# Optimization experiments

Hardware: AMD Instinct MI355X
Metric: run time of the kernel (lower is better)

## Reference

```python
import jax, jax.numpy as jnp
import numpy as np
from jax.nn import relu, softplus, sigmoid

B, T, C, L = 256, 128, 16, 64
ENC, H, OBS_IN, NLAGS = 32, 64, 8, 24
SUBSTEPS = 2


def setup_inputs() -> dict:
    key = jax.random.key(0)
    ks = jax.random.split(key, 32)
    rn = lambda k, shp, s=0.1: jax.random.normal(k, shp, dtype=jnp.float32) * s
    return {
        "timestamps": jnp.linspace(0.0, 1.0, T, dtype=jnp.float32),
        "obs": rn(ks[0], (B, NLAGS, OBS_IN), 1.0),
        "coef_d": rn(ks[1], (B, T - 1, C)),
        "coef_c": rn(ks[2], (B, T - 1, C)),
        "coef_b": rn(ks[3], (B, T - 1, C)),
        "coef_a": rn(ks[4], (B, T - 1, C)),
        "gru_wih": rn(ks[5], (3 * H, OBS_IN)),
        "gru_whh": rn(ks[6], (3 * H, H)),
        "gru_bih": rn(ks[7], (3 * H,)),
        "gru_bhh": rn(ks[8], (3 * H,)),
        "gru_lin_w": rn(ks[9], (ENC, H)),
        "ie_w0": rn(ks[10], (128, ENC + C)),
        "ie_b0": rn(ks[11], (128,)),
        "ie_wh": rn(ks[12], (1, 128, 128)),
        "ie_bh": rn(ks[13], (1, 128)),
        "ie_wout": rn(ks[14], (L, 128)),
        "ie_bout": rn(ks[15], (L,)),
        "vf_w0": rn(ks[16], (128, L)),
        "vf_b0": rn(ks[17], (128,)),
        "vf_wh": rn(ks[18], (1, 128, 128)),
        "vf_bh": rn(ks[19], (1, 128)),
        "vf_wout": rn(ks[20], (L * C, 128)),
        "vf_bout": rn(ks[21], (L * C,)),
        "dec_w0": rn(ks[22], (L // 2, L)),
        "dec_b0": rn(ks[23], (L // 2,)),
        "dec_wh": rn(ks[24], (1, L // 2, L // 2)),
        "dec_bh": rn(ks[25], (1, L // 2)),
        "dec_wout": rn(ks[26], (8, L // 2)),
        "dec_bout": rn(ks[27], (8,)),
    }


def _mlp(x, w0, b0, wh, bh, wout, bout, act, fact):
    h = act(w0 @ x + b0)
    for i in range(wh.shape[0]):  # fixed small depth
        h = act(wh[i] @ h + bh[i])
    return fact(wout @ h + bout)


_ident = lambda v: v


def reference(timestamps, obs, coef_d, coef_c, coef_b, coef_a,
              gru_wih, gru_whh, gru_bih, gru_bhh, gru_lin_w,
              ie_w0, ie_b0, ie_wh, ie_bh, ie_wout, ie_bout,
              vf_w0, vf_b0, vf_wh, vf_bh, vf_wout, vf_bout,
              dec_w0, dec_b0, dec_wh, dec_bh, dec_wout, dec_bout):

    def single(obs_s, d_s, c_s, b_s, a_s):
        # --- GRU observation encoder ---
        def cell(h, x):
            gi = gru_wih @ x + gru_bih
            gh = gru_whh @ h + gru_bhh
            ir, iz, inn = jnp.split(gi, 3)
            hr, hz, hn = jnp.split(gh, 3)
            r = sigmoid(ir + hr)
            z = sigmoid(iz + hz)
            n = jnp.tanh(inn + r * hn)
            return (1.0 - z) * n + z * h, None
        hT, _ = jax.lax.scan(cell, jnp.zeros((H,), jnp.float32), obs_s)
        enc = gru_lin_w @ hT
        # control.evaluate(t0): cubic poly at frac=0 -> constant coeff a[0]
        x0 = a_s[0]
        y0 = _mlp(jnp.concatenate([enc, x0]), ie_w0, ie_b0, ie_wh, ie_bh, ie_wout, ie_bout, relu, _ident)

        def vf(y):
            return _mlp(y, vf_w0, vf_b0, vf_wh, vf_bh, vf_wout, vf_bout, softplus, jnp.tanh).reshape(L, C)

        js = jnp.arange(SUBSTEPS, dtype=jnp.float32)

        def interval(y, xs):
            t0, t1, di, ci, bi = xs
            hstep = (t1 - t0) / SUBSTEPS
            def f(frac, yy):
                dx = bi + 2.0 * ci * frac + 3.0 * di * frac * frac  # dX/dt on this interval
                return vf(yy) @ dx  # (L,)
            def sub(yy, j):  # one fixed Dopri5 step
                f0 = j * hstep
                k1 = f(f0, yy)
                k2 = f(f0 + hstep / 5, yy + hstep * (k1 / 5))
                k3 = f(f0 + 3 * hstep / 10, yy + hstep * (3 / 40 * k1 + 9 / 40 * k2))
                k4 = f(f0 + 4 * hstep / 5, yy + hstep * (44 / 45 * k1 - 56 / 15 * k2 + 32 / 9 * k3))
                k5 = f(f0 + 8 * hstep / 9, yy + hstep * (19372 / 6561 * k1 - 25360 / 2187 * k2 + 64448 / 6561 * k3 - 212 / 729 * k4))
                k6 = f(f0 + hstep, yy + hstep * (9017 / 3168 * k1 - 355 / 33 * k2 + 46732 / 5247 * k3 + 49 / 176 * k4 - 5103 / 18656 * k5))
                yn = yy + hstep * (35 / 384 * k1 + 500 / 1113 * k3 + 125 / 192 * k4 - 2187 / 6784 * k5 + 11 / 84 * k6)
                return yn, None
            y, _ = jax.lax.scan(jax.checkpoint(sub), y, js)
            return y, y

        xs = (timestamps[:-1], timestamps[1:], d_s, c_s, b_s)
        _, ys_rest = jax.lax.scan(interval, y0, xs)
        ys = jnp.concatenate([y0[None], ys_rest], axis=0)  # (T, L)
        dec = lambda yy: _mlp(yy, dec_w0, dec_b0, dec_wh, dec_bh, dec_wout, dec_bout, relu, _ident)
        return jax.vmap(dec)(ys)  # (T, state_size)

    return jax.vmap(single)(obs, coef_d, coef_c, coef_b, coef_a)  # (B, T, state_size)
```

## Files before the change

kernel.cpp:

```cpp
#include <hip/hip_runtime.h>
#include <hip/hip_fp16.h>

#define TPB 512

typedef _Float16 h2v __attribute__((ext_vector_type(2)));

__device__ __forceinline__ float dot2f(unsigned int a, unsigned int b, float c) {
#if __has_builtin(__builtin_amdgcn_fdot2)
    return __builtin_amdgcn_fdot2(__builtin_bit_cast(h2v, a), __builtin_bit_cast(h2v, b), c, false);
#else
    float2 af = __half22float2(__builtin_bit_cast(__half2, a));
    float2 bf = __half22float2(__builtin_bit_cast(__half2, b));
    return fmaf(af.y, bf.y, fmaf(af.x, bf.x, c));
#endif
}

__device__ __forceinline__ unsigned int pack2(float a, float b) {
    unsigned int lo = (unsigned int)__half_as_ushort(__float2half_rn(a));
    unsigned int hi = (unsigned int)__half_as_ushort(__float2half_rn(b));
    return lo | (hi << 16);
}

__device__ __forceinline__ float softplus_f(float x) {
    return fmaxf(x, 0.f) + __logf(1.f + __expf(-fabsf(x)));
}
__device__ __forceinline__ float tanh_f(float x) {
    float e = __expf(2.f * x);
    return 1.f - 2.f / (e + 1.f);
}
__device__ __forceinline__ float sigmoid_f(float x) {
    return 1.f / (1.f + __expf(-x));
}

template <int CTRL>
__device__ __forceinline__ float dpp_add(float x) {
    int m = __builtin_amdgcn_update_dpp(0, __builtin_bit_cast(int, x), CTRL, 0xF, 0xF, true);
    return x + __builtin_bit_cast(float, m);
}

__device__ __forceinline__ float dot16(const float* w, const float* base) {
    float4 a = *reinterpret_cast<const float4*>(base);
    float4 b = *reinterpret_cast<const float4*>(base + 4);
    float4 c = *reinterpret_cast<const float4*>(base + 8);
    float4 d = *reinterpret_cast<const float4*>(base + 12);
    float s0 = w[0] * a.x, s1 = w[1] * a.y, s2 = w[2] * a.z, s3 = w[3] * a.w;
    s0 = fmaf(w[4], b.x, s0);
    s1 = fmaf(w[5], b.y, s1);
    s2 = fmaf(w[6], b.z, s2);
    s3 = fmaf(w[7], b.w, s3);
    s0 = fmaf(w[8], c.x, s0);
    s1 = fmaf(w[9], c.y, s1);
    s2 = fmaf(w[10], c.z, s2);
    s3 = fmaf(w[11], c.w, s3);
    s0 = fmaf(w[12], d.x, s0);
    s1 = fmaf(w[13], d.y, s1);
    s2 = fmaf(w[14], d.z, s2);
    s3 = fmaf(w[15], d.w, s3);
    return (s0 + s1) + (s2 + s3);
}

__global__ __launch_bounds__(TPB, 1) void ncde_kernel(
    const float* __restrict__ timestamps, const float* __restrict__ obs,
    const float* __restrict__ coef_d, const float* __restrict__ coef_c,
    const float* __restrict__ coef_b, const float* __restrict__ coef_a,
    const float* __restrict__ gru_wih, const float* __restrict__ gru_whh,
    const float* __restrict__ gru_bih, const float* __restrict__ gru_bhh,
    const float* __restrict__ gru_lin_w,
    const float* __restrict__ ie_w0, const float* __restrict__ ie_b0,
    const float* __restrict__ ie_wh, const float* __restrict__ ie_bh,
    const float* __restrict__ ie_wout, const float* __restrict__ ie_bout,
    const float* __restrict__ vf_w0, const float* __restrict__ vf_b0,
    const float* __restrict__ vf_wh, const float* __restrict__ vf_bh,
    const float* __restrict__ vf_wout, const float* __restrict__ vf_bout,
    const float* __restrict__ dec_w0, const float* __restrict__ dec_b0,
    const float* __restrict__ dec_wh, const float* __restrict__ dec_bh,
    const float* __restrict__ dec_wout, const float* __restrict__ dec_bout,
    float* __restrict__ out)
{
    const int b = blockIdx.x;
    const int tid = threadIdx.x;

    __shared__ __align__(16) float s_ysall[128][64];
    __shared__ __align__(16) float s_whh[192 * 65];
    __shared__ __align__(16) float s_wih[192 * 9];
    __shared__ __align__(16) float s_obs[24 * 8];
    __shared__ float s_gi[192];
    __shared__ float s_gh[192];
    __shared__ __align__(16) float s_y[64];
    __shared__ __align__(16) __half s_h1h[128];
    __shared__ __align__(16) __half s_h2h[128];
    __shared__ __align__(16) float s_k[6][64];
    __shared__ float s_bi[16], s_ci[16], s_di[16];
    __shared__ __align__(16) float s_v48[48];
    __shared__ float s_m1[128], s_m2[128];

    for (int idx = tid; idx < 192 * 64; idx += TPB)
        s_whh[(idx >> 6) * 65 + (idx & 63)] = gru_whh[idx];
    for (int idx = tid; idx < 192 * 8; idx += TPB)
        s_wih[(idx >> 3) * 9 + (idx & 7)] = gru_wih[idx];
    if (tid < 24 * 8) s_obs[tid] = obs[(size_t)b * 192 + tid];
    const float bih_r = (tid < 192) ? gru_bih[tid] : 0.f;
    const float bhh_r = (tid < 192) ? gru_bhh[tid] : 0.f;
    if (tid < 64) s_y[tid] = 0.f;
    __syncthreads();

    for (int step = 0; step < 24; ++step) {
        if (tid < 192) {
            float gi = bih_r;
            const float* wr = &s_wih[tid * 9];
            const float* xr = &s_obs[step * 8];
#pragma unroll
            for (int j = 0; j < 8; ++j) gi = fmaf(wr[j], xr[j], gi);
            float g0 = bhh_r, g1 = 0.f, g2 = 0.f, g3 = 0.f;
            const float* hr = &s_whh[tid * 65];
#pragma unroll 4
            for (int j = 0; j < 64; j += 4) {
                g0 = fmaf(hr[j + 0], s_y[j + 0], g0);
                g1 = fmaf(hr[j + 1], s_y[j + 1], g1);
                g2 = fmaf(hr[j + 2], s_y[j + 2], g2);
                g3 = fmaf(hr[j + 3], s_y[j + 3], g3);
            }
            s_gi[tid] = gi;
            s_gh[tid] = (g0 + g1) + (g2 + g3);
        }
        __syncthreads();
        if (tid < 64) {
            float rg = sigmoid_f(s_gi[tid] + s_gh[tid]);
            float zg = sigmoid_f(s_gi[64 + tid] + s_gh[64 + tid]);
            float ng = tanh_f(s_gi[128 + tid] + rg * s_gh[128 + tid]);
            s_y[tid] = (1.f - zg) * ng + zg * s_y[tid];
        }
        __syncthreads();
    }

    if (tid < 32) {
        float e = 0.f;
        const float* wr = gru_lin_w + tid * 64;
        for (int j = 0; j < 64; ++j) e = fmaf(wr[j], s_y[j], e);
        s_v48[tid] = e;
    } else if (tid < 48) {
        s_v48[tid] = coef_a[(size_t)b * 127 * 16 + (tid - 32)];
    }
    __syncthreads();

    if (tid < 128) {
        float a = ie_b0[tid];
        const float* wr = ie_w0 + tid * 48;
        for (int j = 0; j < 48; ++j) a = fmaf(wr[j], s_v48[j], a);
        s_m1[tid] = fmaxf(a, 0.f);
    }
    __syncthreads();
    if (tid < 128) {
        float a = ie_bh[tid];
        const float* wr = ie_wh + tid * 128;
        for (int j = 0; j < 128; ++j) a = fmaf(wr[j], s_m1[j], a);
        s_m2[tid] = fmaxf(a, 0.f);
    }
    __syncthreads();
    if (tid < 64) {
        float a = ie_bout[tid];
        const float* wr = ie_wout + tid * 128;
        for (int j = 0; j < 128; ++j) a = fmaf(wr[j], s_m2[j], a);
        s_y[tid] = a;
        s_ysall[0][tid] = a;
    }
    __syncthreads();

    const int row4 = tid >> 2, seg4 = tid & 3;
    float w0_r[16];
    {
        const float* base = vf_w0 + row4 * 64 + seg4 * 16;
#pragma unroll
        for (int j = 0; j < 16; ++j) w0_r[j] = base[j];
    }
    unsigned int wh_r[16];
    {
        const float* base = vf_wh + row4 * 128 + seg4 * 32;
#pragma unroll
        for (int j = 0; j < 16; ++j) wh_r[j] = pack2(base[2 * j], base[2 * j + 1]);
    }
    unsigned int wq0[64], wq1[64];
    {
        const float* r0 = vf_wout + (size_t)(2 * tid) * 128;
#pragma unroll
        for (int j = 0; j < 64; ++j) wq0[j] = pack2(r0[2 * j], r0[2 * j + 1]);
        const float* r1 = r0 + 128;
#pragma unroll
        for (int j = 0; j < 64; ++j) wq1[j] = pack2(r1[2 * j], r1[2 * j + 1]);
    }
    const float b0_r = vf_b0[row4];
    const float bh_r = vf_bh[row4];
    const float bo0 = vf_bout[2 * tid], bo1 = vf_bout[2 * tid + 1];
    const int l_idx = tid >> 3;
    const int c0 = 2 * (tid & 7);

    const size_t cofs = (size_t)b * 127 * 16;

#define VF_STAGE(S, ACC, CC)                                                   \
    do {                                                                       \
        {                                                                      \
            float acc_ = (ACC);                                                \
            acc_ = dpp_add<0xB1>(acc_);                                        \
            acc_ = dpp_add<0x4E>(acc_);                                        \
            if (seg4 == 0) s_h1h[row4] = __float2half_rn(softplus_f(acc_ + b0_r)); \
        }                                                                      \
        __syncthreads();                                                       \
        {                                                                      \
            const __half* hb = &s_h1h[seg4 * 32];                              \
            uint4 h0 = *reinterpret_cast<const uint4*>(hb);                    \
            uint4 h1v = *reinterpret_cast<const uint4*>(hb + 8);               \
            uint4 h2v2 = *reinterpret_cast<const uint4*>(hb + 16);             \
            uint4 h3 = *reinterpret_cast<const uint4*>(hb + 24);               \
            float a0 = dot2f(wh_r[0], h0.x, 0.f);                              \
            float a1 = dot2f(wh_r[1], h0.y, 0.f);                              \
            float a2 = dot2f(wh_r[2], h0.z, 0.f);                              \
            float a3 = dot2f(wh_r[3], h0.w, 0.f);                              \
            a0 = dot2f(wh_r[4], h1v.x, a0);                                    \
            a1 = dot2f(wh_r[5], h1v.y, a1);                                    \
            a2 = dot2f(wh_r[6], h1v.z, a2);                                    \
            a3 = dot2f(wh_r[7], h1v.w, a3);                                    \
            a0 = dot2f(wh_r[8], h2v2.x, a0);                                   \
            a1 = dot2f(wh_r[9], h2v2.y, a1);                                   \
            a2 = dot2f(wh_r[10], h2v2.z, a2);                                  \
            a3 = dot2f(wh_r[11], h2v2.w, a3);                                  \
            a0 = dot2f(wh_r[12], h3.x, a0);                                    \
            a1 = dot2f(wh_r[13], h3.y, a1);                                    \
            a2 = dot2f(wh_r[14], h3.z, a2);                                    \
            a3 = dot2f(wh_r[15], h3.w, a3);                                    \
            float a = (a0 + a1) + (a2 + a3);                                   \
            a = dpp_add<0xB1>(a);                                              \
            a = dpp_add<0x4E>(a);                                              \
            if (seg4 == 0) s_h2h[row4] = __float2half_rn(softplus_f(a + bh_r)); \
        }                                                                      \
        __syncthreads();                                                       \
        {                                                                      \
            float a0 = 0.f, a1 = 0.f, b0a = 0.f, b1a = 0.f;                    \
            _Pragma("unroll")                                                  \
            for (int k4 = 0; k4 < 16; ++k4) {                                  \
                uint4 hv = *reinterpret_cast<const uint4*>(&s_h2h[8 * k4]);    \
                a0 = dot2f(wq0[4 * k4 + 0], hv.x, a0);                         \
                b0a = dot2f(wq1[4 * k4 + 0], hv.x, b0a);                       \
                a1 = dot2f(wq0[4 * k4 + 1], hv.y, a1);                         \
                b1a = dot2f(wq1[4 * k4 + 1], hv.y, b1a);                       \
                a0 = dot2f(wq0[4 * k4 + 2], hv.z, a0);                         \
                b0a = dot2f(wq1[4 * k4 + 2], hv.z, b0a);                       \
                a1 = dot2f(wq0[4 * k4 + 3], hv.w, a1);                         \
                b1a = dot2f(wq1[4 * k4 + 3], hv.w, b1a);                       \
            }                                                                  \
            float v0 = tanh_f(a0 + a1 + bo0);                                  \
            float v1 = tanh_f(b0a + b1a + bo1);                                \
            float frac = fmaf((CC), hstep, f0);                                \
            float dx0 = fmaf(3.f * s_di[c0], frac * frac,                      \
                             fmaf(2.f * s_ci[c0], frac, s_bi[c0]));            \
            float dx1 = fmaf(3.f * s_di[c0 + 1], frac * frac,                  \
                             fmaf(2.f * s_ci[c0 + 1], frac, s_bi[c0 + 1]));    \
            float p = fmaf(v0, dx0, v1 * dx1);                                 \
            p = dpp_add<0xB1>(p);                                              \
            p = dpp_add<0x4E>(p);                                              \
            p = dpp_add<0x141>(p);   \
            if ((tid & 7) == 0) s_k[(S)][l_idx] = p;                           \
        }                                                                      \
        __syncthreads();                                                       \
    } while (0)

#pragma unroll 1
    for (int t = 0; t < 127; ++t) {
        if (tid < 16) s_bi[tid] = coef_b[cofs + t * 16 + tid];
        else if (tid < 32) s_ci[tid - 16] = coef_c[cofs + t * 16 + (tid - 16)];
        else if (tid < 48) s_di[tid - 32] = coef_d[cofs + t * 16 + (tid - 32)];
        const float t0 = timestamps[t], t1 = timestamps[t + 1];
        const float hstep = (t1 - t0) * 0.5f;

#pragma unroll 1
        for (int sub = 0; sub < 2; ++sub) {
            const float f0 = (float)sub * hstep;

            float ay = dot16(w0_r, &s_y[seg4 * 16]);
            VF_STAGE(0, ay, 0.f);
            float dk0 = dot16(w0_r, &s_k[0][seg4 * 16]);
            VF_STAGE(1, fmaf(hstep * 0.2f, dk0, ay), 0.2f);
            float dk1 = dot16(w0_r, &s_k[1][seg4 * 16]);
            VF_STAGE(2, fmaf(hstep, fmaf(3.f / 40.f, dk0, (9.f / 40.f) * dk1), ay), 0.3f);
            float dk2 = dot16(w0_r, &s_k[2][seg4 * 16]);
            VF_STAGE(3, fmaf(hstep, fmaf(44.f / 45.f, dk0,
                          fmaf(-56.f / 15.f, dk1, (32.f / 9.f) * dk2)), ay), 0.8f);
            float dk3 = dot16(w0_r, &s_k[3][seg4 * 16]);
            VF_STAGE(4, fmaf(hstep, fmaf(19372.f / 6561.f, dk0,
                          fmaf(-25360.f / 2187.f, dk1,
                          fmaf(64448.f / 6561.f, dk2, (-212.f / 729.f) * dk3))), ay),
                     8.f / 9.f);
            float dk4 = dot16(w0_r, &s_k[4][seg4 * 16]);
            VF_STAGE(5, fmaf(hstep, fmaf(9017.f / 3168.f, dk0,
                          fmaf(-355.f / 33.f, dk1,
                          fmaf(46732.f / 5247.f, dk2,
                          fmaf(49.f / 176.f, dk3, (-5103.f / 18656.f) * dk4)))), ay),
                     1.f);

            if (tid < 64) {
                float yv = s_y[tid];
                yv = fmaf(hstep * (35.f / 384.f), s_k[0][tid], yv);
                yv = fmaf(hstep * (500.f / 1113.f), s_k[2][tid], yv);
                yv = fmaf(hstep * (125.f / 192.f), s_k[3][tid], yv);
                yv = fmaf(hstep * (-2187.f / 6784.f), s_k[4][tid], yv);
                yv = fmaf(hstep * (11.f / 84.f), s_k[5][tid], yv);
                s_y[tid] = yv;
                if (sub == 1) s_ysall[t + 1][tid] = yv;
            }
            __syncthreads();
        }
    }

    const int wid = tid >> 6, lane = tid & 63;
    for (int t = wid; t < 128; t += 8) {
        const float* yy = s_ysall[t];
        float h1d = 0.f;
        if (lane < 32) {
            float a = dec_b0[lane];
            const float* wr = dec_w0 + lane * 64;
            for (int j = 0; j < 64; ++j) a = fmaf(wr[j], yy[j], a);
            h1d = fmaxf(a, 0.f);
        }
        float a2 = (lane < 32) ? dec_bh[lane] : 0.f;
#pragma unroll 8
        for (int j = 0; j < 32; ++j) {
            float hj = __shfl(h1d, j);
            if (lane < 32) a2 = fmaf(dec_wh[lane * 32 + j], hj, a2);
        }
        float h2d = fmaxf(a2, 0.f);
        float o = (lane < 8) ? dec_bout[lane] : 0.f;
#pragma unroll 8
        for (int j = 0; j < 32; ++j) {
            float hj = __shfl(h2d, j);
            if (lane < 8) o = fmaf(dec_wout[lane * 32 + j], hj, o);
        }
        if (lane < 8) out[(size_t)b * 1024 + t * 8 + lane] = o;
    }
}

extern "C" void kernel_launch(void* const* d_in, const int* in_sizes, int n_in,
                              void* d_out, int out_size, void* d_ws, size_t ws_size,
                              hipStream_t stream) {
    const float* p[29];
    for (int i = 0; i < 29; ++i) p[i] = (const float*)d_in[i];
    ncde_kernel<<<256, TPB, 0, stream>>>(
        p[0], p[1], p[2], p[3], p[4], p[5], p[6], p[7], p[8], p[9], p[10],
        p[11], p[12], p[13], p[14], p[15], p[16], p[17], p[18], p[19], p[20],
        p[21], p[22], p[23], p[24], p[25], p[26], p[27], p[28],
        (float*)d_out);
}
```

Before: 2.293 ms.

## Move half of vf_wout weights to LDS and decode per timestep inline

Half of the packed fp16 vector-field output weights (wq1) now live in a 128KB shared-memory pool instead of registers, reusing the GRU staging area, to cut register pressure and possible spills. The pool aliases the GRU scratch buffers, and the per-interval trajectory buffer is removed; the decoder MLP now runs on wave 0 right after each interval, between the integration steps. This trades register use for an extra LDS load per inner dot-product loop and puts decoder work on the serial critical path.

```diff
diff --git a/kernel.cpp b/kernel.cpp
--- a/kernel.cpp
+++ b/kernel.cpp
@@ -79,20 +79,24 @@
 {
     const int b = blockIdx.x;
     const int tid = threadIdx.x;
-
-    __shared__ __align__(16) float s_ysall[128][64];
-    __shared__ __align__(16) float s_whh[192 * 65];
-    __shared__ __align__(16) float s_wih[192 * 9];
-    __shared__ __align__(16) float s_obs[24 * 8];
-    __shared__ float s_gi[192];
-    __shared__ float s_gh[192];
+    const int lane = tid & 63, wv = tid >> 6;
+
+    __shared__ __align__(16) char s_pool[131072];
+    float* const s_whh = (float*)(s_pool);
+    float* const s_wih = (float*)(s_pool + 49920);
+    float* const s_obs = (float*)(s_pool + 56832);
+    float* const s_gi = (float*)(s_pool + 57600);
+    float* const s_gh = (float*)(s_pool + 58368);
+    float* const s_v48 = (float*)(s_pool + 59136);
+    float* const s_m1 = (float*)(s_pool + 59328);
+    float* const s_m2 = (float*)(s_pool + 59840);
+    unsigned* const s_wq1 = (unsigned*)(s_pool);
+
     __shared__ __align__(16) float s_y[64];
     __shared__ __align__(16) __half s_h1h[128];
     __shared__ __align__(16) __half s_h2h[128];
     __shared__ __align__(16) float s_k[6][64];
     __shared__ float s_bi[16], s_ci[16], s_di[16];
-    __shared__ __align__(16) float s_v48[48];
-    __shared__ float s_m1[128], s_m2[128];
 
     for (int idx = tid; idx < 192 * 64; idx += TPB)
         s_whh[(idx >> 6) * 65 + (idx & 63)] = gru_whh[idx];
@@ -162,7 +166,6 @@
         const float* wr = ie_wout + tid * 128;
         for (int j = 0; j < 128; ++j) a = fmaf(wr[j], s_m2[j], a);
         s_y[tid] = a;
-        s_ysall[0][tid] = a;
     }
     __syncthreads();
 
@@ -179,14 +182,23 @@
 #pragma unroll
         for (int j = 0; j < 16; ++j) wh_r[j] = pack2(base[2 * j], base[2 * j + 1]);
     }
-    unsigned int wq0[64], wq1[64];
+    unsigned int wq0[64];
     {
         const float* r0 = vf_wout + (size_t)(2 * tid) * 128;
 #pragma unroll
         for (int j = 0; j < 64; ++j) wq0[j] = pack2(r0[2 * j], r0[2 * j + 1]);
-        const float* r1 = r0 + 128;
-#pragma unroll
-        for (int j = 0; j < 64; ++j) wq1[j] = pack2(r1[2 * j], r1[2 * j + 1]);
+    }
+    {
+        const float* r1 = vf_wout + (size_t)(2 * tid + 1) * 128;
+#pragma unroll
+        for (int k4 = 0; k4 < 16; ++k4) {
+            uint4 wv1;
+            wv1.x = pack2(r1[8 * k4 + 0], r1[8 * k4 + 1]);
+            wv1.y = pack2(r1[8 * k4 + 2], r1[8 * k4 + 3]);
+            wv1.z = pack2(r1[8 * k4 + 4], r1[8 * k4 + 5]);
+            wv1.w = pack2(r1[8 * k4 + 6], r1[8 * k4 + 7]);
+            *reinterpret_cast<uint4*>(s_wq1 + (size_t)(k4 * 512 + tid) * 4) = wv1;
+        }
     }
     const float b0_r = vf_b0[row4];
     const float bh_r = vf_bh[row4];
@@ -195,6 +207,35 @@
     const int c0 = 2 * (tid & 7);
 
     const size_t cofs = (size_t)b * 127 * 16;
+    __syncthreads();
+
+    auto decode_t = [&](int t) {
+        if (wv == 0) {
+            float h1d = 0.f;
+            if (lane < 32) {
+                float a = dec_b0[lane];
+                const float* wr = dec_w0 + lane * 64;
+#pragma unroll 8
+                for (int j = 0; j < 64; ++j) a = fmaf(wr[j], s_y[j], a);
+                h1d = fmaxf(a, 0.f);
+            }
+            float a2 = (lane < 32) ? dec_bh[lane] : 0.f;
+#pragma unroll 8
+            for (int j = 0; j < 32; ++j) {
+                float hj = __shfl(h1d, j);
+                if (lane < 32) a2 = fmaf(dec_wh[lane * 32 + j], hj, a2);
+            }
+            float h2d = fmaxf(a2, 0.f);
+            float o = (lane < 8) ? dec_bout[lane] : 0.f;
+#pragma unroll 8
+            for (int j = 0; j < 32; ++j) {
+                float hj = __shfl(h2d, j);
+                if (lane < 8) o = fmaf(dec_wout[lane * 32 + j], hj, o);
+            }
+            if (lane < 8) out[(size_t)b * 1024 + t * 8 + lane] = o;
+        }
+    };
+    decode_t(0);
 
 #define VF_STAGE(S, ACC, CC)                                                   \
     do {                                                                       \
@@ -238,14 +279,15 @@
             _Pragma("unroll")                                                  \
             for (int k4 = 0; k4 < 16; ++k4) {                                  \
                 uint4 hv = *reinterpret_cast<const uint4*>(&s_h2h[8 * k4]);    \
+                uint4 wv1 = *reinterpret_cast<const uint4*>(s_wq1 + (k4 * 512 + tid) * 4); \
                 a0 = dot2f(wq0[4 * k4 + 0], hv.x, a0);                         \
-                b0a = dot2f(wq1[4 * k4 + 0], hv.x, b0a);                       \
+                b0a = dot2f(wv1.x, hv.x, b0a);                                 \
                 a1 = dot2f(wq0[4 * k4 + 1], hv.y, a1);                         \
-                b1a = dot2f(wq1[4 * k4 + 1], hv.y, b1a);                       \
+                b1a = dot2f(wv1.y, hv.y, b1a);                                 \
                 a0 = dot2f(wq0[4 * k4 + 2], hv.z, a0);                         \
-                b0a = dot2f(wq1[4 * k4 + 2], hv.z, b0a);                       \
+                b0a = dot2f(wv1.z, hv.z, b0a);                                 \
                 a1 = dot2f(wq0[4 * k4 + 3], hv.w, a1);                         \
-                b1a = dot2f(wq1[4 * k4 + 3], hv.w, b1a);                       \
+                b1a = dot2f(wv1.w, hv.w, b1a);                                 \
             }                                                                  \
             float v0 = tanh_f(a0 + a1 + bo0);                                  \
             float v1 = tanh_f(b0a + b1a + bo1);                                \
@@ -304,36 +346,11 @@
                 yv = fmaf(hstep * (-2187.f / 6784.f), s_k[4][tid], yv);
                 yv = fmaf(hstep * (11.f / 84.f), s_k[5][tid], yv);
                 s_y[tid] = yv;
-                if (sub == 1) s_ysall[t + 1][tid] = yv;
             }
             __syncthreads();
         }
-    }
-
-    const int wid = tid >> 6, lane = tid & 63;
-    for (int t = wid; t < 128; t += 8) {
-        const float* yy = s_ysall[t];
-        float h1d = 0.f;
-        if (lane < 32) {
-            float a = dec_b0[lane];
-            const float* wr = dec_w0 + lane * 64;
-            for (int j = 0; j < 64; ++j) a = fmaf(wr[j], yy[j], a);
-            h1d = fmaxf(a, 0.f);
-        }
-        float a2 = (lane < 32) ? dec_bh[lane] : 0.f;
-#pragma unroll 8
-        for (int j = 0; j < 32; ++j) {
-            float hj = __shfl(h1d, j);
-            if (lane < 32) a2 = fmaf(dec_wh[lane * 32 + j], hj, a2);
-        }
-        float h2d = fmaxf(a2, 0.f);
-        float o = (lane < 8) ? dec_bout[lane] : 0.f;
-#pragma unroll 8
-        for (int j = 0; j < 32; ++j) {
-            float hj = __shfl(h2d, j);
-            if (lane < 8) o = fmaf(dec_wout[lane * 32 + j], hj, o);
-        }
-        if (lane < 8) out[(size_t)b * 1024 + t * 8 + lane] = o;
+
+        decode_t(t + 1);
     }
 }
 
```

After: 2.969 ms. +29.5%, slower.

## Compute vector-field MLP with MFMA matrix cores instead of fp16 dot2 loops

Applied to the files above, without the earlier changes.

Replaces the per-thread fp16 dot2 matrix-vector products in the vector-field MLP with 16x16x32 f16 MFMA instructions. Weights are held in registers as MFMA A-fragments, and the state vector is broadcast as the B operand, so only one column of each result is useful. The first-layer input is now built by a separate phase that forms the RK stage state y+h*sum(k) in half precision, instead of reusing linearity of precomputed dot products. This adds extra barriers and an s_V round trip per stage, and it rounds the first-layer input to fp16, which could cost accuracy.

```diff
diff --git a/kernel.cpp b/kernel.cpp
--- a/kernel.cpp
+++ b/kernel.cpp
@@ -3,23 +3,8 @@
 
 #define TPB 512
 
-typedef _Float16 h2v __attribute__((ext_vector_type(2)));
-
-__device__ __forceinline__ float dot2f(unsigned int a, unsigned int b, float c) {
-#if __has_builtin(__builtin_amdgcn_fdot2)
-    return __builtin_amdgcn_fdot2(__builtin_bit_cast(h2v, a), __builtin_bit_cast(h2v, b), c, false);
-#else
-    float2 af = __half22float2(__builtin_bit_cast(__half2, a));
-    float2 bf = __half22float2(__builtin_bit_cast(__half2, b));
-    return fmaf(af.y, bf.y, fmaf(af.x, bf.x, c));
-#endif
-}
-
-__device__ __forceinline__ unsigned int pack2(float a, float b) {
-    unsigned int lo = (unsigned int)__half_as_ushort(__float2half_rn(a));
-    unsigned int hi = (unsigned int)__half_as_ushort(__float2half_rn(b));
-    return lo | (hi << 16);
-}
+typedef _Float16 f16x8 __attribute__((ext_vector_type(8)));
+typedef float f32x4 __attribute__((ext_vector_type(4)));
 
 __device__ __forceinline__ float softplus_f(float x) {
     return fmaxf(x, 0.f) + __logf(1.f + __expf(-fabsf(x)));
@@ -30,33 +15,16 @@
 }
 __device__ __forceinline__ float sigmoid_f(float x) {
     return 1.f / (1.f + __expf(-x));
+}
+
+__device__ __forceinline__ f32x4 mfma16(f16x8 a, f16x8 b, f32x4 c) {
+    return __builtin_amdgcn_mfma_f32_16x16x32_f16(a, b, c, 0, 0, 0);
 }
 
 template <int CTRL>
 __device__ __forceinline__ float dpp_add(float x) {
     int m = __builtin_amdgcn_update_dpp(0, __builtin_bit_cast(int, x), CTRL, 0xF, 0xF, true);
     return x + __builtin_bit_cast(float, m);
-}
-
-__device__ __forceinline__ float dot16(const float* w, const float* base) {
-    float4 a = *reinterpret_cast<const float4*>(base);
-    float4 b = *reinterpret_cast<const float4*>(base + 4);
-    float4 c = *reinterpret_cast<const float4*>(base + 8);
-    float4 d = *reinterpret_cast<const float4*>(base + 12);
-    float s0 = w[0] * a.x, s1 = w[1] * a.y, s2 = w[2] * a.z, s3 = w[3] * a.w;
-    s0 = fmaf(w[4], b.x, s0);
-    s1 = fmaf(w[5], b.y, s1);
-    s2 = fmaf(w[6], b.z, s2);
-    s3 = fmaf(w[7], b.w, s3);
-    s0 = fmaf(w[8], c.x, s0);
-    s1 = fmaf(w[9], c.y, s1);
-    s2 = fmaf(w[10], c.z, s2);
-    s3 = fmaf(w[11], c.w, s3);
-    s0 = fmaf(w[12], d.x, s0);
-    s1 = fmaf(w[13], d.y, s1);
-    s2 = fmaf(w[14], d.z, s2);
-    s3 = fmaf(w[15], d.w, s3);
-    return (s0 + s1) + (s2 + s3);
 }
 
 __global__ __launch_bounds__(TPB, 1) void ncde_kernel(
@@ -79,6 +47,8 @@
 {
     const int b = blockIdx.x;
     const int tid = threadIdx.x;
+    const int lane = tid & 63, wv = tid >> 6;
+    const int m16 = lane & 15, g4 = lane >> 4;
 
     __shared__ __align__(16) float s_ysall[128][64];
     __shared__ __align__(16) float s_whh[192 * 65];
@@ -87,8 +57,10 @@
     __shared__ float s_gi[192];
     __shared__ float s_gh[192];
     __shared__ __align__(16) float s_y[64];
+    __shared__ __align__(16) __half s_ysbh[64];
     __shared__ __align__(16) __half s_h1h[128];
     __shared__ __align__(16) __half s_h2h[128];
+    __shared__ __align__(16) float s_V[1024];
     __shared__ __align__(16) float s_k[6][64];
     __shared__ float s_bi[16], s_ci[16], s_di[16];
     __shared__ __align__(16) float s_v48[48];
@@ -162,93 +134,122 @@
         const float* wr = ie_wout + tid * 128;
         for (int j = 0; j < 128; ++j) a = fmaf(wr[j], s_m2[j], a);
         s_y[tid] = a;
+        s_ysbh[tid] = __float2half_rn(a);
         s_ysall[0][tid] = a;
     }
     __syncthreads();
 
-    const int row4 = tid >> 2, seg4 = tid & 3;
-    float w0_r[16];
+    f16x8 aw0[2], awh[4], awq[8][4];
     {
-        const float* base = vf_w0 + row4 * 64 + seg4 * 16;
-#pragma unroll
-        for (int j = 0; j < 16; ++j) w0_r[j] = base[j];
-    }
-    unsigned int wh_r[16];
-    {
-        const float* base = vf_wh + row4 * 128 + seg4 * 32;
-#pragma unroll
-        for (int j = 0; j < 16; ++j) wh_r[j] = pack2(base[2 * j], base[2 * j + 1]);
-    }
-    unsigned int wq0[64], wq1[64];
-    {
-        const float* r0 = vf_wout + (size_t)(2 * tid) * 128;
-#pragma unroll
-        for (int j = 0; j < 64; ++j) wq0[j] = pack2(r0[2 * j], r0[2 * j + 1]);
-        const float* r1 = r0 + 128;
-#pragma unroll
-        for (int j = 0; j < 64; ++j) wq1[j] = pack2(r1[2 * j], r1[2 * j + 1]);
-    }
-    const float b0_r = vf_b0[row4];
-    const float bh_r = vf_bh[row4];
+        const int row = wv * 16 + m16;
+#pragma unroll
+        for (int f = 0; f < 2; ++f) {
+            f16x8 a;
+#pragma unroll
+            for (int j = 0; j < 8; ++j)
+                a[j] = (_Float16)vf_w0[row * 64 + f * 32 + g4 * 8 + j];
+            aw0[f] = a;
+        }
+#pragma unroll
+        for (int f = 0; f < 4; ++f) {
+            f16x8 a;
+#pragma unroll
+            for (int j = 0; j < 8; ++j)
+                a[j] = (_Float16)vf_wh[row * 128 + f * 32 + g4 * 8 + j];
+            awh[f] = a;
+        }
+#pragma unroll
+        for (int i = 0; i < 8; ++i) {
+            const int rq = (wv * 8 + i) * 16 + m16;
+#pragma unroll
+            for (int f = 0; f < 4; ++f) {
+                f16x8 a;
+#pragma unroll
+                for (int j = 0; j < 8; ++j)
+                    a[j] = (_Float16)vf_wout[(size_t)rq * 128 + f * 32 + g4 * 8 + j];
+                awq[i][f] = a;
+            }
+        }
+    }
+    const float4 bw0 = *(const float4*)(vf_b0 + wv * 16 + g4 * 4);
+    const float4 bwh = *(const float4*)(vf_bh + wv * 16 + g4 * 4);
     const float bo0 = vf_bout[2 * tid], bo1 = vf_bout[2 * tid + 1];
     const int l_idx = tid >> 3;
     const int c0 = 2 * (tid & 7);
 
     const size_t cofs = (size_t)b * 127 * 16;
 
-#define VF_STAGE(S, ACC, CC)                                                   \
+#define KS(m) s_k[m][tid]
+#define YS_PHASE(...)                                                          \
     do {                                                                       \
-        {                                                                      \
-            float acc_ = (ACC);                                                \
-            acc_ = dpp_add<0xB1>(acc_);                                        \
-            acc_ = dpp_add<0x4E>(acc_);                                        \
-            if (seg4 == 0) s_h1h[row4] = __float2half_rn(softplus_f(acc_ + b0_r)); \
-        }                                                                      \
-        __syncthreads();                                                       \
-        {                                                                      \
-            const __half* hb = &s_h1h[seg4 * 32];                              \
-            uint4 h0 = *reinterpret_cast<const uint4*>(hb);                    \
-            uint4 h1v = *reinterpret_cast<const uint4*>(hb + 8);               \
-            uint4 h2v2 = *reinterpret_cast<const uint4*>(hb + 16);             \
-            uint4 h3 = *reinterpret_cast<const uint4*>(hb + 24);               \
-            float a0 = dot2f(wh_r[0], h0.x, 0.f);                              \
-            float a1 = dot2f(wh_r[1], h0.y, 0.f);                              \
-            float a2 = dot2f(wh_r[2], h0.z, 0.f);                              \
-            float a3 = dot2f(wh_r[3], h0.w, 0.f);                              \
-            a0 = dot2f(wh_r[4], h1v.x, a0);                                    \
-            a1 = dot2f(wh_r[5], h1v.y, a1);                                    \
-            a2 = dot2f(wh_r[6], h1v.z, a2);                                    \
-            a3 = dot2f(wh_r[7], h1v.w, a3);                                    \
-            a0 = dot2f(wh_r[8], h2v2.x, a0);                                   \
-            a1 = dot2f(wh_r[9], h2v2.y, a1);                                   \
-            a2 = dot2f(wh_r[10], h2v2.z, a2);                                  \
-            a3 = dot2f(wh_r[11], h2v2.w, a3);                                  \
-            a0 = dot2f(wh_r[12], h3.x, a0);                                    \
-            a1 = dot2f(wh_r[13], h3.y, a1);                                    \
-            a2 = dot2f(wh_r[14], h3.z, a2);                                    \
-            a3 = dot2f(wh_r[15], h3.w, a3);                                    \
-            float a = (a0 + a1) + (a2 + a3);                                   \
-            a = dpp_add<0xB1>(a);                                              \
-            a = dpp_add<0x4E>(a);                                              \
-            if (seg4 == 0) s_h2h[row4] = __float2half_rn(softplus_f(a + bh_r)); \
-        }                                                                      \
-        __syncthreads();                                                       \
-        {                                                                      \
-            float a0 = 0.f, a1 = 0.f, b0a = 0.f, b1a = 0.f;                    \
+        if (tid < 64) {                                                        \
+            float yv = s_y[tid];                                               \
+            __VA_ARGS__;                                                       \
+            s_ysbh[tid] = __float2half_rn(yv);                                 \
+        }                                                                      \
+        __syncthreads();                                                       \
+    } while (0)
+
+#define MFMA_STAGE(S, CC)                                                      \
+    do {                                                                       \
+        {                          \
+            f16x8 b0 = *(const f16x8*)((const char*)s_ysbh + g4 * 16);         \
+            f16x8 b1 = *(const f16x8*)((const char*)s_ysbh + 64 + g4 * 16);    \
+            f32x4 acc = {0.f, 0.f, 0.f, 0.f};                                  \
+            acc = mfma16(aw0[0], b0, acc);                                     \
+            acc = mfma16(aw0[1], b1, acc);                                     \
+            if (m16 == 0) {                                                    \
+                __half q0 = __float2half_rn(softplus_f(acc[0] + bw0.x));       \
+                __half q1 = __float2half_rn(softplus_f(acc[1] + bw0.y));       \
+                __half q2 = __float2half_rn(softplus_f(acc[2] + bw0.z));       \
+                __half q3 = __float2half_rn(softplus_f(acc[3] + bw0.w));       \
+                uint2 pk;                                                      \
+                pk.x = (unsigned)__half_as_ushort(q0) | ((unsigned)__half_as_ushort(q1) << 16); \
+                pk.y = (unsigned)__half_as_ushort(q2) | ((unsigned)__half_as_ushort(q3) << 16); \
+                *(uint2*)(&s_h1h[wv * 16 + g4 * 4]) = pk;                      \
+            }                                                                  \
+        }                                                                      \
+        __syncthreads();                                                       \
+        {                                                    \
+            f32x4 acc = {0.f, 0.f, 0.f, 0.f};                                  \
             _Pragma("unroll")                                                  \
-            for (int k4 = 0; k4 < 16; ++k4) {                                  \
-                uint4 hv = *reinterpret_cast<const uint4*>(&s_h2h[8 * k4]);    \
-                a0 = dot2f(wq0[4 * k4 + 0], hv.x, a0);                         \
-                b0a = dot2f(wq1[4 * k4 + 0], hv.x, b0a);                       \
-                a1 = dot2f(wq0[4 * k4 + 1], hv.y, a1);                         \
-                b1a = dot2f(wq1[4 * k4 + 1], hv.y, b1a);                       \
-                a0 = dot2f(wq0[4 * k4 + 2], hv.z, a0);                         \
-                b0a = dot2f(wq1[4 * k4 + 2], hv.z, b0a);                       \
-                a1 = dot2f(wq0[4 * k4 + 3], hv.w, a1);                         \
-                b1a = dot2f(wq1[4 * k4 + 3], hv.w, b1a);                       \
+            for (int f = 0; f < 4; ++f) {                                      \
+                f16x8 bf = *(const f16x8*)((const char*)s_h1h + f * 64 + g4 * 16); \
+                acc = mfma16(awh[f], bf, acc);                                 \
             }                                                                  \
-            float v0 = tanh_f(a0 + a1 + bo0);                                  \
-            float v1 = tanh_f(b0a + b1a + bo1);                                \
+            if (m16 == 0) {                                                    \
+                __half q0 = __float2half_rn(softplus_f(acc[0] + bwh.x));       \
+                __half q1 = __float2half_rn(softplus_f(acc[1] + bwh.y));       \
+                __half q2 = __float2half_rn(softplus_f(acc[2] + bwh.z));       \
+                __half q3 = __float2half_rn(softplus_f(acc[3] + bwh.w));       \
+                uint2 pk;                                                      \
+                pk.x = (unsigned)__half_as_ushort(q0) | ((unsigned)__half_as_ushort(q1) << 16); \
+                pk.y = (unsigned)__half_as_ushort(q2) | ((unsigned)__half_as_ushort(q3) << 16); \
+                *(uint2*)(&s_h2h[wv * 16 + g4 * 4]) = pk;                      \
+            }                                                                  \
+        }                                                                      \
+        __syncthreads();                                                       \
+        {                     \
+            f16x8 bf[4];                                                       \
+            _Pragma("unroll")                                                  \
+            for (int f = 0; f < 4; ++f)                                        \
+                bf[f] = *(const f16x8*)((const char*)s_h2h + f * 64 + g4 * 16); \
+            _Pragma("unroll")                                                  \
+            for (int i = 0; i < 8; ++i) {                                      \
+                f32x4 acc = {0.f, 0.f, 0.f, 0.f};                              \
+                acc = mfma16(awq[i][0], bf[0], acc);                           \
+                acc = mfma16(awq[i][1], bf[1], acc);                           \
+                acc = mfma16(awq[i][2], bf[2], acc);                           \
+                acc = mfma16(awq[i][3], bf[3], acc);                           \
+                if (m16 == 0)                                                  \
+                    *(f32x4*)(&s_V[(wv * 8 + i) * 16 + g4 * 4]) = acc;         \
+            }                                                                  \
+        }                                                                      \
+        __syncthreads();                                                       \
+        {              \
+            float2 vp = *(const float2*)(&s_V[l_idx * 16 + c0]);               \
+            float v0 = tanh_f(vp.x + bo0);                                     \
+            float v1 = tanh_f(vp.y + bo1);                                     \
             float frac = fmaf((CC), hstep, f0);                                \
             float dx0 = fmaf(3.f * s_di[c0], frac * frac,                      \
                              fmaf(2.f * s_ci[c0], frac, s_bi[c0]));            \
@@ -257,8 +258,8 @@
             float p = fmaf(v0, dx0, v1 * dx1);                                 \
             p = dpp_add<0xB1>(p);                                              \
             p = dpp_add<0x4E>(p);                                              \
-            p = dpp_add<0x141>(p);   \
-            if ((tid & 7) == 0) s_k[(S)][l_idx] = p;                           \
+            p = dpp_add<0x141>(p);                                             \
+            if ((tid & 7) == 0) s_k[S][l_idx] = p;                             \
         }                                                                      \
         __syncthreads();                                                       \
     } while (0)
@@ -275,26 +276,23 @@
         for (int sub = 0; sub < 2; ++sub) {
             const float f0 = (float)sub * hstep;
 
-            float ay = dot16(w0_r, &s_y[seg4 * 16]);
-            VF_STAGE(0, ay, 0.f);
-            float dk0 = dot16(w0_r, &s_k[0][seg4 * 16]);
-            VF_STAGE(1, fmaf(hstep * 0.2f, dk0, ay), 0.2f);
-            float dk1 = dot16(w0_r, &s_k[1][seg4 * 16]);
-            VF_STAGE(2, fmaf(hstep, fmaf(3.f / 40.f, dk0, (9.f / 40.f) * dk1), ay), 0.3f);
-            float dk2 = dot16(w0_r, &s_k[2][seg4 * 16]);
-            VF_STAGE(3, fmaf(hstep, fmaf(44.f / 45.f, dk0,
-                          fmaf(-56.f / 15.f, dk1, (32.f / 9.f) * dk2)), ay), 0.8f);
-            float dk3 = dot16(w0_r, &s_k[3][seg4 * 16]);
-            VF_STAGE(4, fmaf(hstep, fmaf(19372.f / 6561.f, dk0,
-                          fmaf(-25360.f / 2187.f, dk1,
-                          fmaf(64448.f / 6561.f, dk2, (-212.f / 729.f) * dk3))), ay),
-                     8.f / 9.f);
-            float dk4 = dot16(w0_r, &s_k[4][seg4 * 16]);
-            VF_STAGE(5, fmaf(hstep, fmaf(9017.f / 3168.f, dk0,
-                          fmaf(-355.f / 33.f, dk1,
-                          fmaf(46732.f / 5247.f, dk2,
-                          fmaf(49.f / 176.f, dk3, (-5103.f / 18656.f) * dk4)))), ay),
-                     1.f);
+            MFMA_STAGE(0, 0.f);
+            YS_PHASE(yv = fmaf(hstep * 0.2f, KS(0), yv));
+            MFMA_STAGE(1, 0.2f);
+            YS_PHASE(yv = fmaf(hstep, fmaf(3.f / 40.f, KS(0), (9.f / 40.f) * KS(1)), yv));
+            MFMA_STAGE(2, 0.3f);
+            YS_PHASE(yv = fmaf(hstep, fmaf(44.f / 45.f, KS(0),
+                          fmaf(-56.f / 15.f, KS(1), (32.f / 9.f) * KS(2))), yv));
+            MFMA_STAGE(3, 0.8f);
+            YS_PHASE(yv = fmaf(hstep, fmaf(19372.f / 6561.f, KS(0),
+                          fmaf(-25360.f / 2187.f, KS(1),
+                          fmaf(64448.f / 6561.f, KS(2), (-212.f / 729.f) * KS(3)))), yv));
+            MFMA_STAGE(4, 8.f / 9.f);
+            YS_PHASE(yv = fmaf(hstep, fmaf(9017.f / 3168.f, KS(0),
+                          fmaf(-355.f / 33.f, KS(1),
+                          fmaf(46732.f / 5247.f, KS(2),
+                          fmaf(49.f / 176.f, KS(3), (-5103.f / 18656.f) * KS(4))))), yv));
+            MFMA_STAGE(5, 1.f);
 
             if (tid < 64) {
                 float yv = s_y[tid];
@@ -304,36 +302,37 @@
                 yv = fmaf(hstep * (-2187.f / 6784.f), s_k[4][tid], yv);
                 yv = fmaf(hstep * (11.f / 84.f), s_k[5][tid], yv);
                 s_y[tid] = yv;
+                s_ysbh[tid] = __float2half_rn(yv);
                 if (sub == 1) s_ysall[t + 1][tid] = yv;
             }
             __syncthreads();
         }
     }
 
-    const int wid = tid >> 6, lane = tid & 63;
+    const int wid = tid >> 6, lane2 = tid & 63;
     for (int t = wid; t < 128; t += 8) {
         const float* yy = s_ysall[t];
         float h1d = 0.f;
-        if (lane < 32) {
-            float a = dec_b0[lane];
-            const float* wr = dec_w0 + lane * 64;
+        if (lane2 < 32) {
+            float a = dec_b0[lane2];
+            const float* wr = dec_w0 + lane2 * 64;
             for (int j = 0; j < 64; ++j) a = fmaf(wr[j], yy[j], a);
             h1d = fmaxf(a, 0.f);
         }
-        float a2 = (lane < 32) ? dec_bh[lane] : 0.f;
+        float a2 = (lane2 < 32) ? dec_bh[lane2] : 0.f;
 #pragma unroll 8
         for (int j = 0; j < 32; ++j) {
             float hj = __shfl(h1d, j);
-            if (lane < 32) a2 = fmaf(dec_wh[lane * 32 + j], hj, a2);
+            if (lane2 < 32) a2 = fmaf(dec_wh[lane2 * 32 + j], hj, a2);
         }
         float h2d = fmaxf(a2, 0.f);
-        float o = (lane < 8) ? dec_bout[lane] : 0.f;
+        float o = (lane2 < 8) ? dec_bout[lane2] : 0.f;
 #pragma unroll 8
         for (int j = 0; j < 32; ++j) {
             float hj = __shfl(h2d, j);
-            if (lane < 8) o = fmaf(dec_wout[lane * 32 + j], hj, o);
-        }
-        if (lane < 8) out[(size_t)b * 1024 + t * 8 + lane] = o;
+            if (lane2 < 8) o = fmaf(dec_wout[lane2 * 32 + j], hj, o);
+        }
+        if (lane2 < 8) out[(size_t)b * 1024 + t * 8 + lane2] = o;
     }
 }
 
```

Result: slower. 2.855 ms (+24.5%).

## Compute odd vector-field output rows with MFMA instead of fdot2

Applied to the files above, without the earlier changes.

Half of the 1024-row vf_wout matvec (the odd rows) moves from per-thread fdot2 accumulation to 16x16x32 f16 MFMA, with the hidden vector broadcast as the B operand. Results are written to shared memory and read back after an extra barrier, while even rows stay on the fdot2 path. This cuts per-thread register pressure (64 fewer packed weights) and ALU work, at the cost of an additional __syncthreads per stage and an MFMA that wastes 15 of its 16 columns.

```diff
diff --git a/kernel.cpp b/kernel.cpp
--- a/kernel.cpp
+++ b/kernel.cpp
@@ -4,6 +4,8 @@
 #define TPB 512
 
 typedef _Float16 h2v __attribute__((ext_vector_type(2)));
+typedef _Float16 f16x8 __attribute__((ext_vector_type(8)));
+typedef float f32x4 __attribute__((ext_vector_type(4)));
 
 __device__ __forceinline__ float dot2f(unsigned int a, unsigned int b, float c) {
 #if __has_builtin(__builtin_amdgcn_fdot2)
@@ -30,6 +32,10 @@
 }
 __device__ __forceinline__ float sigmoid_f(float x) {
     return 1.f / (1.f + __expf(-x));
+}
+
+__device__ __forceinline__ f32x4 mfma16(f16x8 a, f16x8 b, f32x4 c) {
+    return __builtin_amdgcn_mfma_f32_16x16x32_f16(a, b, c, 0, 0, 0);
 }
 
 template <int CTRL>
@@ -79,6 +85,8 @@
 {
     const int b = blockIdx.x;
     const int tid = threadIdx.x;
+    const int lane = tid & 63, wv = tid >> 6;
+    const int m16 = lane & 15, g4 = lane >> 4;
 
     __shared__ __align__(16) float s_ysall[128][64];
     __shared__ __align__(16) float s_whh[192 * 65];
@@ -89,6 +97,7 @@
     __shared__ __align__(16) float s_y[64];
     __shared__ __align__(16) __half s_h1h[128];
     __shared__ __align__(16) __half s_h2h[128];
+    __shared__ __align__(16) float s_Vodd[512];
     __shared__ __align__(16) float s_k[6][64];
     __shared__ float s_bi[16], s_ci[16], s_di[16];
     __shared__ __align__(16) float s_v48[48];
@@ -179,14 +188,24 @@
 #pragma unroll
         for (int j = 0; j < 16; ++j) wh_r[j] = pack2(base[2 * j], base[2 * j + 1]);
     }
-    unsigned int wq0[64], wq1[64];
+    unsigned int wq0[64];
     {
         const float* r0 = vf_wout + (size_t)(2 * tid) * 128;
 #pragma unroll
         for (int j = 0; j < 64; ++j) wq0[j] = pack2(r0[2 * j], r0[2 * j + 1]);
-        const float* r1 = r0 + 128;
-#pragma unroll
-        for (int j = 0; j < 64; ++j) wq1[j] = pack2(r1[2 * j], r1[2 * j + 1]);
+    }
+    f16x8 awq[4][4];
+#pragma unroll
+    for (int q = 0; q < 4; ++q) {
+        const int rq = (((wv * 4 + q) * 16 + m16) << 1) | 1;
+#pragma unroll
+        for (int f = 0; f < 4; ++f) {
+            f16x8 a;
+#pragma unroll
+            for (int j = 0; j < 8; ++j)
+                a[j] = (_Float16)vf_wout[(size_t)rq * 128 + f * 32 + g4 * 8 + j];
+            awq[q][f] = a;
+        }
     }
     const float b0_r = vf_b0[row4];
     const float bh_r = vf_bh[row4];
@@ -233,22 +252,53 @@
             if (seg4 == 0) s_h2h[row4] = __float2half_rn(softplus_f(a + bh_r)); \
         }                                                                      \
         __syncthreads();                                                       \
+        float ev_;                                                             \
         {                                                                      \
-            float a0 = 0.f, a1 = 0.f, b0a = 0.f, b1a = 0.f;                    \
+               \
+            f16x8 bf0 = *(const f16x8*)((const char*)s_h2h + 0 * 64 + g4 * 16); \
+            f16x8 bf1 = *(const f16x8*)((const char*)s_h2h + 1 * 64 + g4 * 16); \
+            f16x8 bf2 = *(const f16x8*)((const char*)s_h2h + 2 * 64 + g4 * 16); \
+            f16x8 bf3 = *(const f16x8*)((const char*)s_h2h + 3 * 64 + g4 * 16); \
+            f32x4 q0 = {0.f, 0.f, 0.f, 0.f}, q1 = q0, q2 = q0, q3 = q0;        \
+            q0 = mfma16(awq[0][0], bf0, q0);                                   \
+            q1 = mfma16(awq[1][0], bf0, q1);                                   \
+            q2 = mfma16(awq[2][0], bf0, q2);                                   \
+            q3 = mfma16(awq[3][0], bf0, q3);                                   \
+            q0 = mfma16(awq[0][1], bf1, q0);                                   \
+            q1 = mfma16(awq[1][1], bf1, q1);                                   \
+            q2 = mfma16(awq[2][1], bf1, q2);                                   \
+            q3 = mfma16(awq[3][1], bf1, q3);                                   \
+            q0 = mfma16(awq[0][2], bf2, q0);                                   \
+            q1 = mfma16(awq[1][2], bf2, q1);                                   \
+            q2 = mfma16(awq[2][2], bf2, q2);                                   \
+            q3 = mfma16(awq[3][2], bf2, q3);                                   \
+            q0 = mfma16(awq[0][3], bf3, q0);                                   \
+            q1 = mfma16(awq[1][3], bf3, q1);                                   \
+            q2 = mfma16(awq[2][3], bf3, q2);                                   \
+            q3 = mfma16(awq[3][3], bf3, q3);                                   \
+                    \
+            float a0 = 0.f, a1 = 0.f;                                          \
             _Pragma("unroll")                                                  \
             for (int k4 = 0; k4 < 16; ++k4) {                                  \
                 uint4 hv = *reinterpret_cast<const uint4*>(&s_h2h[8 * k4]);    \
                 a0 = dot2f(wq0[4 * k4 + 0], hv.x, a0);                         \
-                b0a = dot2f(wq1[4 * k4 + 0], hv.x, b0a);                       \
                 a1 = dot2f(wq0[4 * k4 + 1], hv.y, a1);                         \
-                b1a = dot2f(wq1[4 * k4 + 1], hv.y, b1a);                       \
                 a0 = dot2f(wq0[4 * k4 + 2], hv.z, a0);                         \
-                b0a = dot2f(wq1[4 * k4 + 2], hv.z, b0a);                       \
                 a1 = dot2f(wq0[4 * k4 + 3], hv.w, a1);                         \
-                b1a = dot2f(wq1[4 * k4 + 3], hv.w, b1a);                       \
             }                                                                  \
-            float v0 = tanh_f(a0 + a1 + bo0);                                  \
-            float v1 = tanh_f(b0a + b1a + bo1);                                \
+            ev_ = a0 + a1;                                                     \
+                       \
+            if (m16 == 0) {                                                    \
+                *(f32x4*)(&s_Vodd[(wv * 4 + 0) * 16 + g4 * 4]) = q0;           \
+                *(f32x4*)(&s_Vodd[(wv * 4 + 1) * 16 + g4 * 4]) = q1;           \
+                *(f32x4*)(&s_Vodd[(wv * 4 + 2) * 16 + g4 * 4]) = q2;           \
+                *(f32x4*)(&s_Vodd[(wv * 4 + 3) * 16 + g4 * 4]) = q3;           \
+            }                                                                  \
+        }                                                                      \
+        __syncthreads();                                                       \
+        {                                                                      \
+            float v0 = tanh_f(ev_ + bo0);                                      \
+            float v1 = tanh_f(s_Vodd[tid] + bo1);                              \
             float frac = fmaf((CC), hstep, f0);                                \
             float dx0 = fmaf(3.f * s_di[c0], frac * frac,                      \
                              fmaf(2.f * s_ci[c0], frac, s_bi[c0]));            \
@@ -257,7 +307,7 @@
             float p = fmaf(v0, dx0, v1 * dx1);                                 \
             p = dpp_add<0xB1>(p);                                              \
             p = dpp_add<0x4E>(p);                                              \
-            p = dpp_add<0x141>(p);   \
+            p = dpp_add<0x141>(p);           \
             if ((tid & 7) == 0) s_k[(S)][l_idx] = p;                           \
         }                                                                      \
         __syncthreads();                                                       \
@@ -310,30 +360,30 @@
         }
     }
 
-    const int wid = tid >> 6, lane = tid & 63;
+    const int wid = tid >> 6, lane2 = tid & 63;
     for (int t = wid; t < 128; t += 8) {
         const float* yy = s_ysall[t];
         float h1d = 0.f;
-        if (lane < 32) {
-            float a = dec_b0[lane];
-            const float* wr = dec_w0 + lane * 64;
+        if (lane2 < 32) {
+            float a = dec_b0[lane2];
+            const float* wr = dec_w0 + lane2 * 64;
             for (int j = 0; j < 64; ++j) a = fmaf(wr[j], yy[j], a);
             h1d = fmaxf(a, 0.f);
         }
-        float a2 = (lane < 32) ? dec_bh[lane] : 0.f;
+        float a2 = (lane2 < 32) ? dec_bh[lane2] : 0.f;
 #pragma unroll 8
         for (int j = 0; j < 32; ++j) {
             float hj = __shfl(h1d, j);
-            if (lane < 32) a2 = fmaf(dec_wh[lane * 32 + j], hj, a2);
+            if (lane2 < 32) a2 = fmaf(dec_wh[lane2 * 32 + j], hj, a2);
         }
         float h2d = fmaxf(a2, 0.f);
-        float o = (lane < 8) ? dec_bout[lane] : 0.f;
+        float o = (lane2 < 8) ? dec_bout[lane2] : 0.f;
 #pragma unroll 8
         for (int j = 0; j < 32; ++j) {
             float hj = __shfl(h2d, j);
-            if (lane < 8) o = fmaf(dec_wout[lane * 32 + j], hj, o);
-        }
-        if (lane < 8) out[(size_t)b * 1024 + t * 8 + lane] = o;
+            if (lane2 < 8) o = fmaf(dec_wout[lane2 * 32 + j], hj, o);
+        }
+        if (lane2 < 8) out[(size_t)b * 1024 + t * 8 + lane2] = o;
     }
 }
 
```

Measured after the change: 4.027 ms. 75.6% more time.
